# Kernel tuning notes

Measured on AMD Instinct MI355X. Metric: run time of the kernel, lower is better.

The kernel has to match this reference:

```python
import jax, jax.numpy as jnp
import numpy as np

M = 8192            # number of graphs (m)
NODES_PER_GRAPH = 64
N = M * NODES_PER_GRAPH  # total nodes (n)
D_H = 128
D_X = 128


def setup_inputs() -> dict:
    key = jax.random.key(0)
    k1, k2, k3 = jax.random.split(key, 3)
    # scale by 0.1 so the unstabilized exp(e) in segment_softmax stays finite in fp32
    h = 0.1 * jax.random.normal(k1, (M, D_H), dtype=jnp.float32)
    x = 0.1 * jax.random.normal(k2, (N, D_X), dtype=jnp.float32)
    a = jax.random.uniform(k3, (D_H, D_X), dtype=jnp.float32)  # th.rand init
    batch_num_nodes = jnp.full((M,), NODES_PER_GRAPH, dtype=jnp.int32)
    return {"h": h, "x": x, "a": a, "batch_num_nodes": batch_num_nodes}


def reference(h, x, a, batch_num_nodes):
    m = batch_num_nodes.shape[0]
    n = x.shape[0]
    # node -> graph segment ids (repeat_interleave of arange)
    seg = jnp.repeat(jnp.arange(m), batch_num_nodes, total_repeat_length=n)  # (n,)
    ha = (h @ a)[seg]                       # (n, d_x): gather per-graph query to nodes
    e = jnp.sum(x * ha, axis=1)             # (n,) attention logits
    ex = jnp.exp(e)                         # unstabilized exp, faithful to source
    z = jax.ops.segment_sum(ex, seg, num_segments=m)   # (m,) partition functions
    att = ex / z[seg]                       # (n,) segment softmax
    out = jax.ops.segment_sum(att[:, None] * x, seg, num_segments=m)  # (m, d_x)
    return out
```

## Files before the change

kernel.cpp:

```cpp
#include <hip/hip_runtime.h>


#define NPG  64
#define DDIM 128
#define SROW 132

typedef __attribute__((ext_vector_type(4))) float f32x4;

__global__ __launch_bounds__(256) void gat_softmax_kernel(
    const float* __restrict__ h,
    const float* __restrict__ x,
    const float* __restrict__ a,
    float* __restrict__ out)
{
    const int g = blockIdx.x;
    const int t = threadIdx.x;

    __shared__ __align__(16) float xs[NPG * SROW];
    __shared__ float hq[DDIM];
    __shared__ float qpart[2][DDIM];
    __shared__ float q[DDIM];
    __shared__ __align__(16) float epart[256];
    __shared__ float att[NPG];
    __shared__ float opart[2][DDIM];

    const f32x4* xg = reinterpret_cast<const f32x4*>(x + (size_t)g * (NPG * DDIM));
    #pragma unroll
    for (int it = 0; it < 8; ++it) {
        int c = it * 256 + t;
        f32x4 v = xg[c];
        int row = c >> 5;
        int col = c & 31;
        *reinterpret_cast<f32x4*>(&xs[row * SROW + col * 4]) = v;
    }
    if (t < DDIM) hq[t] = h[(size_t)g * DDIM + t];
    __syncthreads();

    {
        const int j    = t & (DDIM - 1);
        const int half = t >> 7;
        const float* ap = a + (size_t)(half * 64) * DDIM + j;
        float acc = 0.f;
        #pragma unroll 16
        for (int k = 0; k < 64; ++k)
            acc += hq[half * 64 + k] * ap[(size_t)k * DDIM];
        qpart[half][j] = acc;
    }
    __syncthreads();
    if (t < DDIM) q[t] = qpart[0][t] + qpart[1][t];
    __syncthreads();

    {
        const int i       = t >> 2;
        const int quarter = t & 3;
        const float* xrow = &xs[i * SROW + quarter * 32];
        const float* qq   = &q[quarter * 32];
        float acc = 0.f;
        #pragma unroll
        for (int c = 0; c < 8; ++c) {
            f32x4 v = *reinterpret_cast<const f32x4*>(xrow + c * 4);
            acc += v[0] * qq[c*4] + v[1] * qq[c*4+1] + v[2] * qq[c*4+2] + v[3] * qq[c*4+3];
        }
        epart[t] = acc;
    }
    __syncthreads();

    if (t < NPG) {
        f32x4 p = *reinterpret_cast<const f32x4*>(&epart[4 * t]);
        float e  = p[0] + p[1] + p[2] + p[3];
        float ex = expf(e);
        float z  = ex;
        #pragma unroll
        for (int m = 32; m >= 1; m >>= 1)
            z += __shfl_xor(z, m, 64);
        att[t] = ex / z;
    }
    __syncthreads();

    {
        const int j   = t & (DDIM - 1);
        const int grp = t >> 7;
        float acc = 0.f;
        #pragma unroll
        for (int k = 0; k < 32; ++k) {
            int i = grp * 32 + k;
            acc += att[i] * xs[i * SROW + j];
        }
        opart[grp][j] = acc;
    }
    __syncthreads();

    if (t < DDIM)
        out[(size_t)g * DDIM + t] = opart[0][t] + opart[1][t];
}

extern "C" void kernel_launch(void* const* d_in, const int* in_sizes, int n_in,
                              void* d_out, int out_size, void* d_ws, size_t ws_size,
                              hipStream_t stream) {
    const float* h = (const float*)d_in[0];
    const float* x = (const float*)d_in[1];
    const float* a = (const float*)d_in[2];
    float* out = (float*)d_out;

    const int m = in_sizes[0] / DDIM;
    gat_softmax_kernel<<<m, 256, 0, stream>>>(h, x, a, out);
}
```

Measured before the change: 374.6 us.

## Split q GEMM into separate kernel and double-buffer x via direct global-to-LDS loads

Moves the h@a query computation into its own kernel that writes q into the output buffer. The main kernel then has each block process 8 graphs in sequence, staging the next graph's x tile and q with global_load_lds into a double-buffered, XOR-swizzled LDS layout while the current graph is being computed. This is meant to overlap memory traffic with compute and to stop reloading the whole matrix a in every block. In exchange it adds a second launch, relies on hand-written vmcnt waits, and reads and writes the same out buffer in place, which is only safe if each graph's q is consumed before its out row is written.

```diff
diff --git a/kernel.cpp b/kernel.cpp
--- a/kernel.cpp
+++ b/kernel.cpp
@@ -1,97 +1,125 @@
 #include <hip/hip_runtime.h>
+#include <stdint.h>
 
 
-#define NPG  64
-#define DDIM 128
-#define SROW 132
+#define NPG   64
+#define DDIM  128
+#define NG    8
 
 typedef __attribute__((ext_vector_type(4))) float f32x4;
 
-__global__ __launch_bounds__(256) void gat_softmax_kernel(
-    const float* __restrict__ h,
-    const float* __restrict__ x,
-    const float* __restrict__ a,
-    float* __restrict__ out)
+__device__ __forceinline__ void gld_lds16(const void* g, void* l) {
+    __builtin_amdgcn_global_load_lds(
+        (const __attribute__((address_space(1))) void*)g,
+        (__attribute__((address_space(3))) void*)l,
+        16, 0, 0);
+}
+
+__global__ __launch_bounds__(256) void q_gemm(const float* __restrict__ h,
+                                              const float* __restrict__ a,
+                                              float* __restrict__ q)
 {
-    const int g = blockIdx.x;
-    const int t = threadIdx.x;
+    const int t    = threadIdx.x;
+    const int j    = t & (DDIM - 1);
+    const int half = t >> 7;
+    const size_t g0 = (size_t)blockIdx.x * 8 + (size_t)half * 4;
+    const float* hg = h + g0 * DDIM;
+    const float* ac = a + j;
+    float a0 = 0.f, a1 = 0.f, a2 = 0.f, a3 = 0.f;
+    #pragma unroll 8
+    for (int k = 0; k < DDIM; ++k) {
+        const float av = ac[(size_t)k * DDIM];
+        a0 += hg[k]          * av;
+        a1 += hg[DDIM   + k] * av;
+        a2 += hg[2*DDIM + k] * av;
+        a3 += hg[3*DDIM + k] * av;
+    }
+    q[(g0 + 0) * DDIM + j] = a0;
+    q[(g0 + 1) * DDIM + j] = a1;
+    q[(g0 + 2) * DDIM + j] = a2;
+    q[(g0 + 3) * DDIM + j] = a3;
+}
 
-    __shared__ __align__(16) float xs[NPG * SROW];
-    __shared__ float hq[DDIM];
-    __shared__ float qpart[2][DDIM];
-    __shared__ float q[DDIM];
-    __shared__ __align__(16) float epart[256];
-    __shared__ float att[NPG];
-    __shared__ float opart[2][DDIM];
+__global__ __launch_bounds__(256) void gat_main(const float* __restrict__ x,
+                                                const float* qsrc,
+                                                float* out)
+{
+    __shared__ __align__(16) float xs[2][NPG * DDIM];
+    __shared__ __align__(16) float qs[2][DDIM];
+    __shared__ float ep[256];
 
-    const f32x4* xg = reinterpret_cast<const f32x4*>(x + (size_t)g * (NPG * DDIM));
-    #pragma unroll
-    for (int it = 0; it < 8; ++it) {
-        int c = it * 256 + t;
-        f32x4 v = xg[c];
-        int row = c >> 5;
-        int col = c & 31;
-        *reinterpret_cast<f32x4*>(&xs[row * SROW + col * 4]) = v;
-    }
-    if (t < DDIM) hq[t] = h[(size_t)g * DDIM + t];
-    __syncthreads();
+    const int t    = threadIdx.x;
+    const int lane = t & 63;
+    const int w    = t >> 6;
+    const int l5   = lane >> 5;
+    const int g0   = blockIdx.x * NG;
 
-    {
-        const int j    = t & (DDIM - 1);
-        const int half = t >> 7;
-        const float* ap = a + (size_t)(half * 64) * DDIM + j;
-        float acc = 0.f;
-        #pragma unroll 16
-        for (int k = 0; k < 64; ++k)
-            acc += hq[half * 64 + k] * ap[(size_t)k * DDIM];
-        qpart[half][j] = acc;
-    }
-    __syncthreads();
-    if (t < DDIM) q[t] = qpart[0][t] + qpart[1][t];
-    __syncthreads();
+    auto stage = [&](int g, int b) {
+        const char* xg = (const char*)(x + (size_t)g * (NPG * DDIM));
+        #pragma unroll
+        for (int it = 0; it < 8; ++it) {
+            const int Lbase = (w * 8 + it) * 64;
+            const int K     = ((2 * it) & 7) | l5;
+            gld_lds16(xg + (size_t)(Lbase + (lane ^ K)) * 16,
+                      (char*)&xs[b][0] + (size_t)Lbase * 16);
+        }
+        if (lane < 32)
+            gld_lds16((const char*)(qsrc + (size_t)g * DDIM) + lane * 16,
+                      (char*)&qs[b][0]);
+    };
 
-    {
-        const int i       = t >> 2;
-        const int quarter = t & 3;
-        const float* xrow = &xs[i * SROW + quarter * 32];
-        const float* qq   = &q[quarter * 32];
+    stage(g0, 0);
+
+    #pragma unroll 1
+    for (int gi = 0; gi < NG; ++gi) {
+        const int cur = gi & 1;
+        const int g   = g0 + gi;
+
+        if (gi + 1 < NG) {
+            stage(g0 + gi + 1, cur ^ 1);
+            asm volatile("s_waitcnt vmcnt(9)" ::: "memory");
+        } else {
+            asm volatile("s_waitcnt vmcnt(0)" ::: "memory");
+        }
+        __builtin_amdgcn_s_barrier();
+
+        const float* xb = &xs[cur][0];
+        const float* qw = &qs[cur][w * 32];
+        const int rowbase = lane * 32 + w * 8;
+        const int ia7     = lane & 7;
         float acc = 0.f;
         #pragma unroll
         for (int c = 0; c < 8; ++c) {
-            f32x4 v = *reinterpret_cast<const f32x4*>(xrow + c * 4);
-            acc += v[0] * qq[c*4] + v[1] * qq[c*4+1] + v[2] * qq[c*4+2] + v[3] * qq[c*4+3];
+            const f32x4 v = *(const f32x4*)(xb + (size_t)(rowbase + (c ^ ia7)) * 4);
+            acc += v[0]*qw[c*4+0] + v[1]*qw[c*4+1] + v[2]*qw[c*4+2] + v[3]*qw[c*4+3];
         }
-        epart[t] = acc;
+        ep[t] = acc;
+        asm volatile("s_waitcnt lgkmcnt(0)" ::: "memory");
+        __builtin_amdgcn_s_barrier();
+
+        const float e  = ep[lane] + ep[64 + lane] + ep[128 + lane] + ep[192 + lane];
+        const float ex = expf(e);
+        float z = ex;
+        #pragma unroll
+        for (int m = 32; m >= 1; m >>= 1) z += __shfl_xor(z, m, 64);
+        const float att = ex / z;
+
+        if (t < DDIM) {
+            const int jc = t >> 2, jd = t & 3;
+            float o0 = 0.f, o1 = 0.f;
+            #pragma unroll
+            for (int i = 0; i < NPG; i += 2) {
+                const float w0 = __shfl(att, i,     64);
+                const float w1 = __shfl(att, i + 1, 64);
+                o0 += w0 * xb[(size_t)(((i    ) * 32 + jc) ^ ((i    ) & 7)) * 4 + jd];
+                o1 += w1 * xb[(size_t)(((i + 1) * 32 + jc) ^ ((i + 1) & 7)) * 4 + jd];
+            }
+            out[(size_t)g * DDIM + t] = o0 + o1;
+        }
+        asm volatile("" ::: "memory");
+        __builtin_amdgcn_s_barrier();
+        asm volatile("" ::: "memory");
     }
-    __syncthreads();
-
-    if (t < NPG) {
-        f32x4 p = *reinterpret_cast<const f32x4*>(&epart[4 * t]);
-        float e  = p[0] + p[1] + p[2] + p[3];
-        float ex = expf(e);
-        float z  = ex;
-        #pragma unroll
-        for (int m = 32; m >= 1; m >>= 1)
-            z += __shfl_xor(z, m, 64);
-        att[t] = ex / z;
-    }
-    __syncthreads();
-
-    {
-        const int j   = t & (DDIM - 1);
-        const int grp = t >> 7;
-        float acc = 0.f;
-        #pragma unroll
-        for (int k = 0; k < 32; ++k) {
-            int i = grp * 32 + k;
-            acc += att[i] * xs[i * SROW + j];
-        }
-        opart[grp][j] = acc;
-    }
-    __syncthreads();
-
-    if (t < DDIM)
-        out[(size_t)g * DDIM + t] = opart[0][t] + opart[1][t];
 }
 
 extern "C" void kernel_launch(void* const* d_in, const int* in_sizes, int n_in,
@@ -103,5 +131,6 @@
     float* out = (float*)d_out;
 
     const int m = in_sizes[0] / DDIM;
-    gat_softmax_kernel<<<m, 256, 0, stream>>>(h, x, a, out);
+    q_gemm<<<m / 8, 256, 0, stream>>>(h, a, out);
+    gat_main<<<m / NG, 256, 0, stream>>>(x, out, out);
 }
```

Result: slower. 390.3 us (+4.2%).
